# Optimization experiments

Measured on AMD Instinct MI355X. Metric: run time of the kernel, lower is better.

Reference implementation:

```python
import jax, jax.numpy as jnp
import numpy as np

B, D, S = 4096, 1024, 1024

def setup_inputs() -> dict:
    key = jax.random.key(0)
    ks = jax.random.split(key, 12)
    u = lambda k, shp: jax.random.uniform(k, shp, jnp.float32, -0.05, 0.05)
    return {
        "inputs": jax.random.normal(ks[0], (B, D), jnp.float32),
        "h0": jax.random.normal(ks[1], (B, S), jnp.float32),
        "c0": jax.random.normal(ks[2], (B, S), jnp.float32),
        "w_f": u(ks[3], (D, S)), "u_f": u(ks[4], (S, S)), "b_f": u(ks[5], (S,)),
        "w_i": u(ks[6], (D, S)), "u_i": u(ks[7], (S, S)), "b_i": u(ks[8], (S,)),
        "w_o": u(ks[9], (D, S)), "u_o": u(ks[10], (S, S)), "b_o": u(ks[11], (S,)),
    }

def reference(inputs, h0, c0, w_f, u_f, b_f, w_i, u_i, b_i, w_o, u_o, b_o):
    # Faithful to the original: input_cell reuses the FORGET gate weights and
    # sigmoid (not tanh, not w_c) -- a quirk of the source module.
    pre_f = inputs @ w_f + h0 @ u_f + b_f          # [B, S]
    forget_gate = jax.nn.sigmoid(pre_f)
    input_gate = jax.nn.sigmoid(inputs @ w_i + h0 @ u_i + b_i)
    output_gate = jax.nn.sigmoid(inputs @ w_o + h0 @ u_o + b_o)
    input_cell = jax.nn.sigmoid(pre_f)             # same pre-activation as forget gate
    c_new = forget_gate * c0 + input_cell * input_gate
    h_new = output_gate * jnp.tanh(c_new)
    return (h_new, c_new)
```

## Files before the change

kernel.cpp:

```cpp
#include <hip/hip_runtime.h>
#include <cstdint>
#include <cstddef>


typedef __attribute__((ext_vector_type(8))) short bf16x8;
typedef __attribute__((ext_vector_type(4))) float f32x4;
typedef __attribute__((ext_vector_type(8))) short s16x8;
typedef __attribute__((ext_vector_type(4))) float f32x4v;

#define MROWS 4096
#define KD    1024
#define KALL  2048
#define NC    1024

__device__ __forceinline__ short f2bf(float f) {
    uint32_t u = __builtin_bit_cast(uint32_t, f);
    u += 0x7fffu + ((u >> 16) & 1u);
    return (short)(u >> 16);
}

__global__ void cvt_bf16_kernel(const float* __restrict__ x,
                                const float* __restrict__ h,
                                short* __restrict__ ab) {
    int b = blockIdx.x;
    const float* in;
    int coff;
    if (b < 2048) { in = x; coff = 0; }
    else          { in = h; coff = KD; b -= 2048; }
    const int i = (b * 256 + threadIdx.x) * 8;
    const int row = i >> 10, col = i & 1023;
    f32x4v a = *(const f32x4v*)(in + i);
    f32x4v c = *(const f32x4v*)(in + i + 4);
    s16x8 o;
    o[0] = f2bf(a[0]); o[1] = f2bf(a[1]); o[2] = f2bf(a[2]); o[3] = f2bf(a[3]);
    o[4] = f2bf(c[0]); o[5] = f2bf(c[1]); o[6] = f2bf(c[2]); o[7] = f2bf(c[3]);
    *(s16x8*)(ab + (size_t)row * KALL + coff + col) = o;
}

struct W6 { const float* src[6]; };

__global__ void pack_w_kernel(W6 p, short* __restrict__ bp) {
    __shared__ short tile[32][33];
    const int z = blockIdx.z;
    const float* __restrict__ w = p.src[z];
    const int g    = (z < 3) ? z : z - 3;
    const int koff = (z < 3) ? 0 : KD;
    const int tx = threadIdx.x & 31;
    const int ty = threadIdx.x >> 5;
    const int kbase = blockIdx.y * 32;
    const int nbase = blockIdx.x * 32;
#pragma unroll
    for (int r = 0; r < 4; ++r) {
        int k = kbase + ty + r * 8;
        tile[ty + r * 8][tx] = f2bf(w[k * NC + nbase + tx]);
    }
    __syncthreads();
#pragma unroll
    for (int r = 0; r < 4; ++r) {
        const int n = nbase + ty + r * 8;
        const int pcol = ((n >> 4) * 3 + g) * 16 + (n & 15);
        bp[(size_t)pcol * KALL + koff + kbase + tx] = tile[tx][ty + r * 8];
    }
}

__global__ __launch_bounds__(512, 2)
void lstm_gemm_kernel(const short* __restrict__ Ab, const short* __restrict__ Bp,
                      const float* __restrict__ bf_, const float* __restrict__ bi_,
                      const float* __restrict__ bo_,
                      const float* __restrict__ c0,
                      float* __restrict__ outH, float* __restrict__ outC) {
    __shared__ __align__(16) char lds[2][57344];

    const int tid  = threadIdx.x;
    const int lane = tid & 63;
    const int wave = tid >> 6;
    const int wr   = wave >> 1;
    const int wc   = wave & 1;
    const int m0   = blockIdx.y * 256;
    const int np0  = blockIdx.x * 192;

    const int l15 = lane & 15;
    const int q   = lane >> 4;

    f32x4 acc[4][2][3] = {};

    const int srow = tid >> 2;
    const int skel = ((tid & 3) ^ ((tid >> 3) & 3)) * 8;
    const short* aPtr[4];
#pragma unroll
    for (int l = 0; l < 4; ++l) {
        const int ks = l >> 1, mh = l & 1;
        aPtr[l] = Ab + (size_t)(m0 + mh * 128 + srow) * KALL + ks * 32 + skel;
    }
    const short* bPtr[3];
#pragma unroll
    for (int w = 0; w < 3; ++w) {
        const int pbyte = w * 8192 + tid * 16;
        const int ks  = pbyte / 12288;
        const int rem = pbyte - ks * 12288;
        const int row = rem >> 6;
        const int slot = (rem >> 4) & 3;
        bPtr[w] = Bp + (size_t)(np0 + row) * KALL + ks * 32 +
                  ((slot ^ ((row >> 1) & 3)) * 8);
    }

    int aOffV[4];
#pragma unroll
    for (int m = 0; m < 4; ++m) {
        const int r = wr * 64 + m * 16 + l15;
        const int r1 = r & 127;
        aOffV[m] = (r >> 7) * 8192 + r1 * 64 + ((q ^ ((r1 >> 1) & 3)) << 4);
    }
    int bOffV[2][3];
#pragma unroll
    for (int nt = 0; nt < 2; ++nt)
#pragma unroll
        for (int g = 0; g < 3; ++g) {
            const int rb = (wc * 2 + nt) * 48 + g * 16 + l15;
            bOffV[nt][g] = 32768 + rb * 64 + ((q ^ ((rb >> 1) & 3)) << 4);
        }

#define GLDS(SRC, DOFF)                                                      \
    __builtin_amdgcn_global_load_lds(                                        \
        (const __attribute__((address_space(1))) unsigned int*)(uintptr_t)(SRC), \
        (__attribute__((address_space(3))) unsigned int*)(uintptr_t)         \
            (Ls + (DOFF) + tid * 16), 16, 0, 0)

#define BAR    __builtin_amdgcn_s_barrier()
#define SCHED0 __builtin_amdgcn_sched_barrier(0)
#define LGKM0  asm volatile("s_waitcnt lgkmcnt(0)" ::: "memory")
#define WAITV(N) asm volatile("s_waitcnt vmcnt(" #N ")" ::: "memory")

#define MFMA24(AF, BG)                                                       \
    {                                                                        \
        __builtin_amdgcn_s_setprio(1);                                       \
        _Pragma("unroll")                                                    \
        for (int mm = 0; mm < 4; ++mm)                                       \
            _Pragma("unroll")                                                \
            for (int nt = 0; nt < 2; ++nt)                                   \
                _Pragma("unroll")                                            \
                for (int g = 0; g < 3; ++g)                                  \
                    acc[mm][nt][g] = __builtin_amdgcn_mfma_f32_16x16x32_bf16(\
                        AF[mm], BG[nt][g], acc[mm][nt][g], 0, 0, 0);         \
        __builtin_amdgcn_s_setprio(0);                                       \
    }

    {
        char* Ls = lds[0];
        GLDS(aPtr[0], 0);      GLDS(aPtr[1], 8192);
        GLDS(bPtr[0], 32768);  GLDS(bPtr[1], 40960);
        GLDS(aPtr[2], 16384);  GLDS(aPtr[3], 24576);
        GLDS(bPtr[2], 49152);
    }

    bf16x8 af[4], bg[2][3];

    for (int t = 0; t < 31; ++t) {
        const char* L = lds[t & 1];
        char* Ls = lds[(t + 1) & 1];
        const int kb = (t + 1) * 64;

        WAITV(3);
        BAR;
        SCHED0;
#pragma unroll
        for (int mm = 0; mm < 4; ++mm) af[mm] = *(const bf16x8*)(L + aOffV[mm]);
#pragma unroll
        for (int nt = 0; nt < 2; ++nt)
#pragma unroll
            for (int g = 0; g < 3; ++g)
                bg[nt][g] = *(const bf16x8*)(L + bOffV[nt][g]);
        GLDS(aPtr[0] + kb, 0);
        GLDS(aPtr[1] + kb, 8192);
        GLDS(bPtr[0] + kb, 32768);
        GLDS(bPtr[1] + kb, 40960);
        SCHED0;
        LGKM0;
        SCHED0;
        MFMA24(af, bg);

        WAITV(4);
        BAR;
        SCHED0;
#pragma unroll
        for (int mm = 0; mm < 4; ++mm)
            af[mm] = *(const bf16x8*)(L + 16384 + aOffV[mm]);
#pragma unroll
        for (int nt = 0; nt < 2; ++nt)
#pragma unroll
            for (int g = 0; g < 3; ++g)
                bg[nt][g] = *(const bf16x8*)(L + 12288 + bOffV[nt][g]);
        GLDS(aPtr[2] + kb, 16384);
        GLDS(aPtr[3] + kb, 24576);
        GLDS(bPtr[2] + kb, 49152);
        SCHED0;
        LGKM0;
        SCHED0;
        MFMA24(af, bg);
    }

    {
        const char* L = lds[1];
        WAITV(3);
        BAR;
        SCHED0;
#pragma unroll
        for (int mm = 0; mm < 4; ++mm) af[mm] = *(const bf16x8*)(L + aOffV[mm]);
#pragma unroll
        for (int nt = 0; nt < 2; ++nt)
#pragma unroll
            for (int g = 0; g < 3; ++g)
                bg[nt][g] = *(const bf16x8*)(L + bOffV[nt][g]);
        LGKM0;
        SCHED0;
        MFMA24(af, bg);

        WAITV(0);
        BAR;
        SCHED0;
#pragma unroll
        for (int mm = 0; mm < 4; ++mm)
            af[mm] = *(const bf16x8*)(L + 16384 + aOffV[mm]);
#pragma unroll
        for (int nt = 0; nt < 2; ++nt)
#pragma unroll
            for (int g = 0; g < 3; ++g)
                bg[nt][g] = *(const bf16x8*)(L + 12288 + bOffV[nt][g]);
        LGKM0;
        SCHED0;
        MFMA24(af, bg);
    }

    const int rj = q * 4;
#pragma unroll
    for (int m = 0; m < 4; ++m) {
#pragma unroll
        for (int nt = 0; nt < 2; ++nt) {
            const int col = blockIdx.x * 64 + (wc * 2 + nt) * 16 + l15;
            const float bfv = bf_[col], biv = bi_[col], bov = bo_[col];
            const f32x4 pf = acc[m][nt][0];
            const f32x4 pi = acc[m][nt][1];
            const f32x4 po = acc[m][nt][2];
#pragma unroll
            for (int j = 0; j < 4; ++j) {
                const int row = m0 + wr * 64 + m * 16 + rj + j;
                const float fg = 1.f / (1.f + __expf(-(pf[j] + bfv)));
                const float ig = 1.f / (1.f + __expf(-(pi[j] + biv)));
                const float og = 1.f / (1.f + __expf(-(po[j] + bov)));
                const float cv = c0[row * NC + col];
                const float cn = fg * cv + fg * ig;
                const float e  = __expf(-2.f * cn);
                const float th = (1.f - e) / (1.f + e);
                outH[row * NC + col] = og * th;
                outC[row * NC + col] = cn;
            }
        }
    }
#undef GLDS
#undef BAR
#undef SCHED0
#undef LGKM0
#undef WAITV
#undef MFMA24
}

extern "C" void kernel_launch(void* const* d_in, const int* in_sizes, int n_in,
                              void* d_out, int out_size, void* d_ws, size_t ws_size,
                              hipStream_t stream) {
    const float* inputs = (const float*)d_in[0];
    const float* h0     = (const float*)d_in[1];
    const float* c0     = (const float*)d_in[2];
    const float* w_f    = (const float*)d_in[3];
    const float* u_f    = (const float*)d_in[4];
    const float* b_f    = (const float*)d_in[5];
    const float* w_i    = (const float*)d_in[6];
    const float* u_i    = (const float*)d_in[7];
    const float* b_i    = (const float*)d_in[8];
    const float* w_o    = (const float*)d_in[9];
    const float* u_o    = (const float*)d_in[10];
    const float* b_o    = (const float*)d_in[11];

    float* outH = (float*)d_out;
    float* outC = outH + (size_t)MROWS * NC;

    char* ws = (char*)d_ws;
    short* Ab = (short*)(ws);
    short* Bp = (short*)(ws + (16u << 20));

    cvt_bf16_kernel<<<4096, 256, 0, stream>>>(inputs, h0, Ab);

    W6 p;
    p.src[0] = w_f; p.src[1] = w_i; p.src[2] = w_o;
    p.src[3] = u_f; p.src[4] = u_i; p.src[5] = u_o;
    pack_w_kernel<<<dim3(32, 32, 6), 256, 0, stream>>>(p, Bp);

    dim3 grid(16, 16);
    lstm_gemm_kernel<<<grid, 512, 0, stream>>>(
        Ab, Bp, b_f, b_i, b_o, c0, outH, outC);
}
```

Before: 73.09 us.

## Switch GEMM to 32x32x16 bf16 MFMA with 32-column gate-interleaved weight packing

Replaces the 16x16x32 MFMA tiling (24 instructions per half-step) with 32x32x16 MFMA (12 per half-step). The weight packing interleaves gates in 32-column groups instead of 16, and the LDS fragment offsets and epilogue row mapping are rewritten to match. The aim is fewer LDS fragment reads per MFMA and a denser matrix instruction. The swizzled LDS reads may now hit bank conflicts, and the epilogue writes 32 contiguous columns per row, which changes global store coalescing.

```diff
diff --git a/kernel.cpp b/kernel.cpp
--- a/kernel.cpp
+++ b/kernel.cpp
@@ -4,7 +4,7 @@
 
 
 typedef __attribute__((ext_vector_type(8))) short bf16x8;
-typedef __attribute__((ext_vector_type(4))) float f32x4;
+typedef __attribute__((ext_vector_type(16))) float f32x16;
 typedef __attribute__((ext_vector_type(8))) short s16x8;
 typedef __attribute__((ext_vector_type(4))) float f32x4v;
 
@@ -58,7 +58,7 @@
 #pragma unroll
     for (int r = 0; r < 4; ++r) {
         const int n = nbase + ty + r * 8;
-        const int pcol = ((n >> 4) * 3 + g) * 16 + (n & 15);
+        const int pcol = ((n >> 5) * 3 + g) * 32 + (n & 31);
         bp[(size_t)pcol * KALL + koff + kbase + tx] = tile[tx][ty + r * 8];
     }
 }
@@ -79,10 +79,10 @@
     const int m0   = blockIdx.y * 256;
     const int np0  = blockIdx.x * 192;
 
-    const int l15 = lane & 15;
-    const int q   = lane >> 4;
-
-    f32x4 acc[4][2][3] = {};
+    const int l31  = lane & 31;
+    const int half = lane >> 5;
+
+    f32x16 acc[2][3] = {};
 
     const int srow = tid >> 2;
     const int skel = ((tid & 3) ^ ((tid >> 3) & 3)) * 8;
@@ -104,20 +104,24 @@
                   ((slot ^ ((row >> 1) & 3)) * 8);
     }
 
-    int aOffV[4];
-#pragma unroll
-    for (int m = 0; m < 4; ++m) {
-        const int r = wr * 64 + m * 16 + l15;
-        const int r1 = r & 127;
-        aOffV[m] = (r >> 7) * 8192 + r1 * 64 + ((q ^ ((r1 >> 1) & 3)) << 4);
-    }
-    int bOffV[2][3];
-#pragma unroll
-    for (int nt = 0; nt < 2; ++nt)
-#pragma unroll
-        for (int g = 0; g < 3; ++g) {
-            const int rb = (wc * 2 + nt) * 48 + g * 16 + l15;
-            bOffV[nt][g] = 32768 + rb * 64 + ((q ^ ((rb >> 1) & 3)) << 4);
+    int aOffV[2][2];
+#pragma unroll
+    for (int mf = 0; mf < 2; ++mf)
+#pragma unroll
+        for (int kc = 0; kc < 2; ++kc) {
+            const int r  = wr * 64 + mf * 32 + l31;
+            const int r1 = r & 127;
+            aOffV[mf][kc] = (r >> 7) * 8192 + r1 * 64 +
+                            (((kc * 2 + half) ^ ((r1 >> 1) & 3)) << 4);
+        }
+    int bOffV[3][2];
+#pragma unroll
+    for (int g = 0; g < 3; ++g)
+#pragma unroll
+        for (int kc = 0; kc < 2; ++kc) {
+            const int rb = wc * 96 + g * 32 + l31;
+            bOffV[g][kc] = 32768 + rb * 64 +
+                           (((kc * 2 + half) ^ ((rb >> 1) & 3)) << 4);
         }
 
 #define GLDS(SRC, DOFF)                                                      \
@@ -131,18 +135,18 @@
 #define LGKM0  asm volatile("s_waitcnt lgkmcnt(0)" ::: "memory")
 #define WAITV(N) asm volatile("s_waitcnt vmcnt(" #N ")" ::: "memory")
 
-#define MFMA24(AF, BG)                                                       \
-    {                                                                        \
-        __builtin_amdgcn_s_setprio(1);                                       \
-        _Pragma("unroll")                                                    \
-        for (int mm = 0; mm < 4; ++mm)                                       \
-            _Pragma("unroll")                                                \
-            for (int nt = 0; nt < 2; ++nt)                                   \
-                _Pragma("unroll")                                            \
-                for (int g = 0; g < 3; ++g)                                  \
-                    acc[mm][nt][g] = __builtin_amdgcn_mfma_f32_16x16x32_bf16(\
-                        AF[mm], BG[nt][g], acc[mm][nt][g], 0, 0, 0);         \
-        __builtin_amdgcn_s_setprio(0);                                       \
+#define MFMA12(AF, BG)                                                      \
+    {                                                                       \
+        __builtin_amdgcn_s_setprio(1);                                      \
+        _Pragma("unroll")                                                   \
+        for (int kc = 0; kc < 2; ++kc)                                      \
+            _Pragma("unroll")                                               \
+            for (int mf = 0; mf < 2; ++mf)                                  \
+                _Pragma("unroll")                                           \
+                for (int g = 0; g < 3; ++g)                                 \
+                    acc[mf][g] = __builtin_amdgcn_mfma_f32_32x32x16_bf16(   \
+                        AF[mf][kc], BG[g][kc], acc[mf][g], 0, 0, 0);        \
+        __builtin_amdgcn_s_setprio(0);                                      \
     }
 
     {
@@ -153,7 +157,7 @@
         GLDS(bPtr[2], 49152);
     }
 
-    bf16x8 af[4], bg[2][3];
+    bf16x8 af[2][2], bg[3][2];
 
     for (int t = 0; t < 31; ++t) {
         const char* L = lds[t & 1];
@@ -164,12 +168,15 @@
         BAR;
         SCHED0;
 #pragma unroll
-        for (int mm = 0; mm < 4; ++mm) af[mm] = *(const bf16x8*)(L + aOffV[mm]);
-#pragma unroll
-        for (int nt = 0; nt < 2; ++nt)
-#pragma unroll
-            for (int g = 0; g < 3; ++g)
-                bg[nt][g] = *(const bf16x8*)(L + bOffV[nt][g]);
+        for (int mf = 0; mf < 2; ++mf)
+#pragma unroll
+            for (int kc = 0; kc < 2; ++kc)
+                af[mf][kc] = *(const bf16x8*)(L + aOffV[mf][kc]);
+#pragma unroll
+        for (int g = 0; g < 3; ++g)
+#pragma unroll
+            for (int kc = 0; kc < 2; ++kc)
+                bg[g][kc] = *(const bf16x8*)(L + bOffV[g][kc]);
         GLDS(aPtr[0] + kb, 0);
         GLDS(aPtr[1] + kb, 8192);
         GLDS(bPtr[0] + kb, 32768);
@@ -177,26 +184,28 @@
         SCHED0;
         LGKM0;
         SCHED0;
-        MFMA24(af, bg);
+        MFMA12(af, bg);
 
         WAITV(4);
         BAR;
         SCHED0;
 #pragma unroll
-        for (int mm = 0; mm < 4; ++mm)
-            af[mm] = *(const bf16x8*)(L + 16384 + aOffV[mm]);
-#pragma unroll
-        for (int nt = 0; nt < 2; ++nt)
-#pragma unroll
-            for (int g = 0; g < 3; ++g)
-                bg[nt][g] = *(const bf16x8*)(L + 12288 + bOffV[nt][g]);
+        for (int mf = 0; mf < 2; ++mf)
+#pragma unroll
+            for (int kc = 0; kc < 2; ++kc)
+                af[mf][kc] = *(const bf16x8*)(L + 16384 + aOffV[mf][kc]);
+#pragma unroll
+        for (int g = 0; g < 3; ++g)
+#pragma unroll
+            for (int kc = 0; kc < 2; ++kc)
+                bg[g][kc] = *(const bf16x8*)(L + 12288 + bOffV[g][kc]);
         GLDS(aPtr[2] + kb, 16384);
         GLDS(aPtr[3] + kb, 24576);
         GLDS(bPtr[2] + kb, 49152);
         SCHED0;
         LGKM0;
         SCHED0;
-        MFMA24(af, bg);
+        MFMA12(af, bg);
     }
 
     {
@@ -205,55 +214,57 @@
         BAR;
         SCHED0;
 #pragma unroll
-        for (int mm = 0; mm < 4; ++mm) af[mm] = *(const bf16x8*)(L + aOffV[mm]);
-#pragma unroll
-        for (int nt = 0; nt < 2; ++nt)
-#pragma unroll
-            for (int g = 0; g < 3; ++g)
-                bg[nt][g] = *(const bf16x8*)(L + bOffV[nt][g]);
+        for (int mf = 0; mf < 2; ++mf)
+#pragma unroll
+            for (int kc = 0; kc < 2; ++kc)
+                af[mf][kc] = *(const bf16x8*)(L + aOffV[mf][kc]);
+#pragma unroll
+        for (int g = 0; g < 3; ++g)
+#pragma unroll
+            for (int kc = 0; kc < 2; ++kc)
+                bg[g][kc] = *(const bf16x8*)(L + bOffV[g][kc]);
         LGKM0;
         SCHED0;
-        MFMA24(af, bg);
+        MFMA12(af, bg);
 
         WAITV(0);
         BAR;
         SCHED0;
 #pragma unroll
-        for (int mm = 0; mm < 4; ++mm)
-            af[mm] = *(const bf16x8*)(L + 16384 + aOffV[mm]);
-#pragma unroll
-        for (int nt = 0; nt < 2; ++nt)
-#pragma unroll
-            for (int g = 0; g < 3; ++g)
-                bg[nt][g] = *(const bf16x8*)(L + 12288 + bOffV[nt][g]);
+        for (int mf = 0; mf < 2; ++mf)
+#pragma unroll
+            for (int kc = 0; kc < 2; ++kc)
+                af[mf][kc] = *(const bf16x8*)(L + 16384 + aOffV[mf][kc]);
+#pragma unroll
+        for (int g = 0; g < 3; ++g)
+#pragma unroll
+            for (int kc = 0; kc < 2; ++kc)
+                bg[g][kc] = *(const bf16x8*)(L + 12288 + bOffV[g][kc]);
         LGKM0;
         SCHED0;
-        MFMA24(af, bg);
-    }
-
-    const int rj = q * 4;
-#pragma unroll
-    for (int m = 0; m < 4; ++m) {
-#pragma unroll
-        for (int nt = 0; nt < 2; ++nt) {
-            const int col = blockIdx.x * 64 + (wc * 2 + nt) * 16 + l15;
-            const float bfv = bf_[col], biv = bi_[col], bov = bo_[col];
-            const f32x4 pf = acc[m][nt][0];
-            const f32x4 pi = acc[m][nt][1];
-            const f32x4 po = acc[m][nt][2];
-#pragma unroll
-            for (int j = 0; j < 4; ++j) {
-                const int row = m0 + wr * 64 + m * 16 + rj + j;
-                const float fg = 1.f / (1.f + __expf(-(pf[j] + bfv)));
-                const float ig = 1.f / (1.f + __expf(-(pi[j] + biv)));
-                const float og = 1.f / (1.f + __expf(-(po[j] + bov)));
-                const float cv = c0[row * NC + col];
-                const float cn = fg * cv + fg * ig;
-                const float e  = __expf(-2.f * cn);
-                const float th = (1.f - e) / (1.f + e);
-                outH[row * NC + col] = og * th;
-                outC[row * NC + col] = cn;
-            }
+        MFMA12(af, bg);
+    }
+
+    const int col = blockIdx.x * 64 + wc * 32 + l31;
+    const float bfv = bf_[col], biv = bi_[col], bov = bo_[col];
+#pragma unroll
+    for (int mf = 0; mf < 2; ++mf) {
+        const f32x16 pf = acc[mf][0];
+        const f32x16 pi = acc[mf][1];
+        const f32x16 po = acc[mf][2];
+#pragma unroll
+        for (int j = 0; j < 16; ++j) {
+            const int row = m0 + wr * 64 + mf * 32 +
+                            (j & 3) + 8 * (j >> 2) + 4 * half;
+            const float fg = 1.f / (1.f + __expf(-(pf[j] + bfv)));
+            const float ig = 1.f / (1.f + __expf(-(pi[j] + biv)));
+            const float og = 1.f / (1.f + __expf(-(po[j] + bov)));
+            const float cv = c0[row * NC + col];
+            const float cn = fg * cv + fg * ig;
+            const float e  = __expf(-2.f * cn);
+            const float th = (1.f - e) / (1.f + e);
+            outH[row * NC + col] = og * th;
+            outC[row * NC + col] = cn;
         }
     }
 #undef GLDS
@@ -261,7 +272,7 @@
 #undef SCHED0
 #undef LGKM0
 #undef WAITV
-#undef MFMA24
+#undef MFMA12
 }
 
 extern "C" void kernel_launch(void* const* d_in, const int* in_sizes, int n_in,
```

Result: slower. 78.39 us (+7.3%).
